# Kernel optimization log

Hardware: AMD Instinct MI355X
Metric: run time of the kernel (lower is better)

## Reference

```python
import jax, jax.numpy as jnp
import numpy as np

N_USER, N_ITEM = 100000, 50000
D, H, B, E = 64, 64, 16384, 2000000

def _xavier(key, shape):
    fan_in, fan_out = shape[0], shape[1]
    lim = float(np.sqrt(6.0 / (fan_in + fan_out)))
    return jax.random.uniform(key, shape, jnp.float32, -lim, lim)

def setup_inputs() -> dict:
    key = jax.random.key(0)
    ks = jax.random.split(key, 16)
    inp = {
        "user_table": _xavier(ks[0], (N_USER, D)),
        "item_table": _xavier(ks[1], (N_ITEM, D)),
        "Wu": _xavier(ks[2], (D, D)),   # GCN_user weight ([in,out])
        "bu": jnp.zeros((D,), jnp.float32),
        "Wi": _xavier(ks[3], (D, D)),   # GCN_item weight
        "bi": jnp.zeros((D,), jnp.float32),
        "W1": _xavier(ks[4], (4 * D, 2 * H)),
        "b1": jnp.zeros((2 * H,), jnp.float32),
        "W2": _xavier(ks[5], (2 * H, H)),
        "b2": jnp.zeros((H,), jnp.float32),
        "W3": _xavier(ks[6], (H, 1)),
        "b3": jnp.zeros((1,), jnp.float32),
        "user_bias": jnp.zeros((N_USER, 1), jnp.float32),
        "item_bias": jnp.zeros((N_ITEM, 1), jnp.float32),
        "user_id": jax.random.randint(ks[7], (B,), 0, N_USER),
        "item_id": jax.random.randint(ks[8], (B,), 0, N_ITEM),
        "edge_user": jax.random.randint(ks[9], (E,), 0, N_USER),
        "edge_item": jax.random.randint(ks[10], (E,), 0, N_ITEM),
    }
    return inp

def reference(user_table, item_table, Wu, bu, Wi, bi, W1, b1, W2, b2, W3, b3,
              user_bias, item_bias, user_id, item_id, edge_user, edge_item):
    # sparse.mm(edge_ui, item_h)[user_id]: aggregate item embeddings per user
    agg_i = jax.ops.segment_sum(item_table[edge_item], edge_user, num_segments=N_USER)[user_id]
    agg_u = jax.ops.segment_sum(user_table[edge_user], edge_item, num_segments=N_ITEM)[item_id]
    ones_e = jnp.ones((edge_user.shape[0],), jnp.float32)
    deg_u = jax.ops.segment_sum(ones_e, edge_user, num_segments=N_USER)[user_id] + 1.0  # item_din
    deg_i = jax.ops.segment_sum(ones_e, edge_item, num_segments=N_ITEM)[item_id] + 1.0  # user_din
    gcn_item_h = agg_i / deg_u[:, None]   # [B, D]
    gcn_user_h = agg_u / deg_i[:, None]   # [B, D]
    # dropout p=0.3 is identity in eval mode
    gcn_user_out = jax.nn.relu(gcn_user_h @ Wu + bu)
    gcn_item_out = jax.nn.relu(gcn_item_h @ Wi + bi)
    u_emb = user_table[user_id]
    i_emb = item_table[item_id]
    x = jnp.concatenate([u_emb * i_emb,
                         u_emb * gcn_item_out,
                         gcn_user_out * i_emb,
                         gcn_user_out * gcn_item_out], axis=-1)  # [B, 4D]
    x1 = jnp.tanh(x @ W1 + b1)
    x2 = jnp.tanh(x1 @ W2 + b2)
    x3 = (x2 @ W3 + b3).reshape(-1)
    return x3 + user_bias[user_id, 0] + item_bias[item_id, 0]
```

## Files before the change

### kernel.cpp

```cpp
#include <hip/hip_runtime.h>
#include <cstdint>
#include <cstddef>

#define D 64
#define CAPU 96
#define CAPI 128
#define OCAP 4096
#define GR 32

__global__ __launch_bounds__(256) void k_build_maps(const int* __restrict__ user_id,
                                                    const int* __restrict__ item_id,
                                                    int* __restrict__ map_u,
                                                    int* __restrict__ map_i, int B)
{
    int i = blockIdx.x * blockDim.x + threadIdx.x;
    if (i < B) {
        atomicCAS(&map_u[user_id[i]], -1, i);
        atomicCAS(&map_i[item_id[i]], -1, i);
    }
}

__global__ __launch_bounds__(256) void k_scatter(const int* __restrict__ edge_user,
                                                 const int* __restrict__ edge_item,
                                                 const int* __restrict__ map_u,
                                                 const int* __restrict__ map_i,
                                                 int* __restrict__ cntU,
                                                 int* __restrict__ cntI,
                                                 uint32_t* __restrict__ listU,
                                                 uint32_t* __restrict__ listI,
                                                 int* __restrict__ ovfCnt,
                                                 uint32_t* __restrict__ ovf, int E)
{
    int t = blockIdx.x * blockDim.x + threadIdx.x;
    int base = t * 2;
    if (base >= E) return;

    int u0, u1 = -1, i0, i1 = 0;
    if (base + 2 <= E) {
        int2 eu = *(const int2*)(edge_user + base);
        int2 ei = *(const int2*)(edge_item + base);
        u0 = eu.x; u1 = eu.y; i0 = ei.x; i1 = ei.y;
    } else {
        u0 = edge_user[base]; i0 = edge_item[base];
    }

    int su0 = map_u[u0];
    int si0 = map_i[i0];
    int su1 = (u1 >= 0) ? map_u[u1] : -1;
    int si1 = (u1 >= 0) ? map_i[i1] : -1;

    if (su0 >= 0) {
        int pos = atomicAdd(&cntU[su0 * 16], 1);
        if (pos < CAPU) listU[(size_t)su0 * CAPU + pos] = (uint32_t)i0;
        else { int o = atomicAdd(ovfCnt, 1);
               if (o < OCAP) ovf[o] = ((uint32_t)su0 << 17) | (uint32_t)i0; }
    }
    if (si0 >= 0) {
        int pos = atomicAdd(&cntI[si0 * 16], 1);
        if (pos < CAPI) listI[(size_t)si0 * CAPI + pos] = (uint32_t)u0;
        else { int o = atomicAdd(ovfCnt, 1);
               if (o < OCAP) ovf[o] = 0x80000000u | ((uint32_t)si0 << 17) | (uint32_t)u0; }
    }
    if (su1 >= 0) {
        int pos = atomicAdd(&cntU[su1 * 16], 1);
        if (pos < CAPU) listU[(size_t)su1 * CAPU + pos] = (uint32_t)i1;
        else { int o = atomicAdd(ovfCnt, 1);
               if (o < OCAP) ovf[o] = ((uint32_t)su1 << 17) | (uint32_t)i1; }
    }
    if (si1 >= 0) {
        int pos = atomicAdd(&cntI[si1 * 16], 1);
        if (pos < CAPI) listI[(size_t)si1 * CAPI + pos] = (uint32_t)u1;
        else { int o = atomicAdd(ovfCnt, 1);
               if (o < OCAP) ovf[o] = 0x80000000u | ((uint32_t)si1 << 17) | (uint32_t)u1; }
    }
}

__global__ __launch_bounds__(256) void k_gather(const uint32_t* __restrict__ listU,
                                                const uint32_t* __restrict__ listI,
                                                const int* __restrict__ cntU,
                                                const int* __restrict__ cntI,
                                                const float* __restrict__ user_table,
                                                const float* __restrict__ item_table,
                                                const int* __restrict__ ovfCnt,
                                                const uint32_t* __restrict__ ovf,
                                                float* __restrict__ aggIU,
                                                float* __restrict__ aggUI, int B)
{
    int gg = (blockIdx.x * blockDim.x + threadIdx.x) >> 4;
    if (gg >= 2 * B) return;
    int l16 = threadIdx.x & 15;
    int side = gg >= B;
    int slot = side ? gg - B : gg;

    int cnt = side ? cntI[slot * 16] : cntU[slot * 16];
    int caps = side ? CAPI : CAPU;
    int n = cnt < caps ? cnt : caps;
    const uint32_t* list = side ? (listI + (size_t)slot * CAPI)
                                : (listU + (size_t)slot * CAPU);
    const float4* table4 = (const float4*)(side ? user_table : item_table);

    float4 a0 = {0.f,0.f,0.f,0.f}, a1 = {0.f,0.f,0.f,0.f};
    float4 a2 = {0.f,0.f,0.f,0.f}, a3 = {0.f,0.f,0.f,0.f};
    int j = 0;
    for (; j + 4 <= n; j += 4) {
        int r0 = (int)list[j], r1 = (int)list[j+1], r2 = (int)list[j+2], r3 = (int)list[j+3];
        float4 v0 = table4[(size_t)r0 * 16 + l16];
        float4 v1 = table4[(size_t)r1 * 16 + l16];
        float4 v2 = table4[(size_t)r2 * 16 + l16];
        float4 v3 = table4[(size_t)r3 * 16 + l16];
        a0.x += v0.x; a0.y += v0.y; a0.z += v0.z; a0.w += v0.w;
        a1.x += v1.x; a1.y += v1.y; a1.z += v1.z; a1.w += v1.w;
        a2.x += v2.x; a2.y += v2.y; a2.z += v2.z; a2.w += v2.w;
        a3.x += v3.x; a3.y += v3.y; a3.z += v3.z; a3.w += v3.w;
    }
    for (; j < n; ++j) {
        int r0 = (int)list[j];
        float4 v0 = table4[(size_t)r0 * 16 + l16];
        a0.x += v0.x; a0.y += v0.y; a0.z += v0.z; a0.w += v0.w;
    }
    if (cnt > caps) {
        int on = *ovfCnt; if (on > OCAP) on = OCAP;
        for (int k = 0; k < on; ++k) {
            uint32_t p = ovf[k];
            if ((int)(p >> 31) == side && (int)((p >> 17) & 0x3FFFu) == slot) {
                float4 v = table4[(size_t)(p & 0x1FFFFu) * 16 + l16];
                a0.x += v.x; a0.y += v.y; a0.z += v.z; a0.w += v.w;
            }
        }
    }
    float inv = 1.0f / ((float)cnt + 1.0f);
    float4 acc = {(a0.x+a1.x+a2.x+a3.x) * inv, (a0.y+a1.y+a2.y+a3.y) * inv,
                  (a0.z+a1.z+a2.z+a3.z) * inv, (a0.w+a1.w+a2.w+a3.w) * inv};
    float4* agg4 = (float4*)(side ? aggUI : aggIU);
    agg4[(size_t)slot * 16 + l16] = acc;
}

__global__ __launch_bounds__(256) void k_gcn_mlp(const int* __restrict__ user_id,
                                                 const int* __restrict__ item_id,
                                                 const int* __restrict__ map_u,
                                                 const int* __restrict__ map_i,
                                                 const float* __restrict__ aggIU,
                                                 const float* __restrict__ aggUI,
                                                 const float* __restrict__ user_table,
                                                 const float* __restrict__ item_table,
                                                 const float* __restrict__ Wi,
                                                 const float* __restrict__ bi,
                                                 const float* __restrict__ Wu,
                                                 const float* __restrict__ bu,
                                                 const float* __restrict__ W1,
                                                 const float* __restrict__ b1,
                                                 const float* __restrict__ W2,
                                                 const float* __restrict__ b2,
                                                 const float* __restrict__ W3,
                                                 const float* __restrict__ b3,
                                                 const float* __restrict__ user_bias,
                                                 const float* __restrict__ item_bias,
                                                 float* __restrict__ out, int B)
{
    __shared__ float XgiL[GR][68];
    __shared__ float XguL[GR][68];
    __shared__ float Fbuf[2 * GR][68];
    __shared__ float WB[8192];
    __shared__ int sU[GR], sI[GR];
    int t = threadIdx.x;
    int row0 = blockIdx.x * GR;
    if (t < GR) { sU[t] = user_id[row0 + t]; sI[t] = item_id[row0 + t]; }
    __syncthreads();

    int txg = t & 15, tyg = t >> 4;
    {
        const float4* agg4 = (const float4*)aggIU;
        #pragma unroll
        for (int q = 0; q < 2; ++q) {
            int idx = t * 2 + q; int r = idx >> 4, l16 = idx & 15;
            int slot = map_u[sU[r]];
            ((float4*)&Fbuf[r][0])[l16] = agg4[(size_t)slot * 16 + l16];
        }
        const float4* wg = (const float4*)Wi;
        float4* d = (float4*)WB;
        #pragma unroll
        for (int q = 0; q < 4; ++q) d[t + q * 256] = wg[t + q * 256];
    }
    __syncthreads();
    {
        float acc[2][4] = {};
        for (int k = 0; k < 64; ++k) {
            float a0 = Fbuf[2 * tyg][k], a1 = Fbuf[2 * tyg + 1][k];
            #pragma unroll
            for (int c = 0; c < 4; ++c) {
                float w = WB[k * 64 + txg + 16 * c];
                acc[0][c] = fmaf(a0, w, acc[0][c]);
                acc[1][c] = fmaf(a1, w, acc[1][c]);
            }
        }
        #pragma unroll
        for (int r = 0; r < 2; ++r)
            #pragma unroll
            for (int c = 0; c < 4; ++c)
                XgiL[2 * tyg + r][txg + 16 * c] = fmaxf(acc[r][c] + bi[txg + 16 * c], 0.f);
    }
    __syncthreads();
    {
        const float4* agg4 = (const float4*)aggUI;
        #pragma unroll
        for (int q = 0; q < 2; ++q) {
            int idx = t * 2 + q; int r = idx >> 4, l16 = idx & 15;
            int slot = map_i[sI[r]];
            ((float4*)&Fbuf[r][0])[l16] = agg4[(size_t)slot * 16 + l16];
        }
        const float4* wg = (const float4*)Wu;
        float4* d = (float4*)WB;
        #pragma unroll
        for (int q = 0; q < 4; ++q) d[t + q * 256] = wg[t + q * 256];
    }
    __syncthreads();
    {
        float acc[2][4] = {};
        for (int k = 0; k < 64; ++k) {
            float a0 = Fbuf[2 * tyg][k], a1 = Fbuf[2 * tyg + 1][k];
            #pragma unroll
            for (int c = 0; c < 4; ++c) {
                float w = WB[k * 64 + txg + 16 * c];
                acc[0][c] = fmaf(a0, w, acc[0][c]);
                acc[1][c] = fmaf(a1, w, acc[1][c]);
            }
        }
        #pragma unroll
        for (int r = 0; r < 2; ++r)
            #pragma unroll
            for (int c = 0; c < 4; ++c)
                XguL[2 * tyg + r][txg + 16 * c] = fmaxf(acc[r][c] + bu[txg + 16 * c], 0.f);
    }
    __syncthreads();

    #pragma unroll
    for (int q = 0; q < 2; ++q) {
        int idx = t * 2 + q; int r = idx >> 4, l16 = idx & 15;
        ((float4*)&Fbuf[r][0])[l16] = ((const float4*)user_table)[(size_t)sU[r] * 16 + l16];
        ((float4*)&Fbuf[GR + r][0])[l16] = ((const float4*)item_table)[(size_t)sI[r] * 16 + l16];
    }

    int tx1 = t & 31, ty1 = t >> 5;
    float acc1[4][4] = {};
    for (int j = 0; j < 4; ++j) {
        {
            const float4* w4 = (const float4*)W1 + (size_t)j * 2048;
            float4* d = (float4*)WB;
            #pragma unroll
            for (int q = 0; q < 8; ++q) d[t + q * 256] = w4[t + q * 256];
        }
        __syncthreads();
        const float (*FA)[68] = (j < 2) ? (const float (*)[68])&Fbuf[0] : (const float (*)[68])XguL;
        const float (*FB)[68] = ((j & 1) == 0) ? (const float (*)[68])&Fbuf[GR] : (const float (*)[68])XgiL;
        for (int k = 0; k < 64; ++k) {
            float a[4], b[4];
            #pragma unroll
            for (int r = 0; r < 4; ++r) a[r] = FA[4 * ty1 + r][k] * FB[4 * ty1 + r][k];
            #pragma unroll
            for (int c = 0; c < 4; ++c) b[c] = WB[k * 128 + tx1 + 32 * c];
            #pragma unroll
            for (int r = 0; r < 4; ++r)
                #pragma unroll
                for (int c = 0; c < 4; ++c)
                    acc1[r][c] = fmaf(a[r], b[c], acc1[r][c]);
        }
        __syncthreads();
    }

    float* x1t = &Fbuf[0][0];
    #pragma unroll
    for (int r = 0; r < 4; ++r)
        #pragma unroll
        for (int c = 0; c < 4; ++c) {
            int col = tx1 + 32 * c;
            x1t[(4 * ty1 + r) * 132 + col] = tanhf(acc1[r][c] + b1[col]);
        }
    {
        const float4* w4 = (const float4*)W2;
        float4* d = (float4*)WB;
        #pragma unroll
        for (int q = 0; q < 8; ++q) d[t + q * 256] = w4[t + q * 256];
    }
    __syncthreads();

    int tx2 = t & 15, ty2 = t >> 4;
    float acc2[2][4] = {};
    for (int k = 0; k < 128; ++k) {
        float a0 = x1t[(2 * ty2) * 132 + k];
        float a1 = x1t[(2 * ty2 + 1) * 132 + k];
        #pragma unroll
        for (int c = 0; c < 4; ++c) {
            float w = WB[k * 64 + tx2 + 16 * c];
            acc2[0][c] = fmaf(a0, w, acc2[0][c]);
            acc2[1][c] = fmaf(a1, w, acc2[1][c]);
        }
    }
    float b3v = b3[0];
    #pragma unroll
    for (int r = 0; r < 2; ++r) {
        int lr = 2 * ty2 + r;
        float p = 0.f;
        #pragma unroll
        for (int c = 0; c < 4; ++c) {
            int col = tx2 + 16 * c;
            p += tanhf(acc2[r][c] + b2[col]) * W3[col];
        }
        p += __shfl_xor(p, 1);
        p += __shfl_xor(p, 2);
        p += __shfl_xor(p, 4);
        p += __shfl_xor(p, 8);
        if (tx2 == 0)
            out[row0 + lr] = p + b3v + user_bias[sU[lr]] + item_bias[sI[lr]];
    }
}

extern "C" void kernel_launch(void* const* d_in, const int* in_sizes, int n_in,
                              void* d_out, int out_size, void* d_ws, size_t ws_size,
                              hipStream_t stream)
{
    const float* user_table = (const float*)d_in[0];
    const float* item_table = (const float*)d_in[1];
    const float* Wu = (const float*)d_in[2];
    const float* bu = (const float*)d_in[3];
    const float* Wi = (const float*)d_in[4];
    const float* bi = (const float*)d_in[5];
    const float* W1 = (const float*)d_in[6];
    const float* b1 = (const float*)d_in[7];
    const float* W2 = (const float*)d_in[8];
    const float* b2 = (const float*)d_in[9];
    const float* W3 = (const float*)d_in[10];
    const float* b3 = (const float*)d_in[11];
    const float* user_bias = (const float*)d_in[12];
    const float* item_bias = (const float*)d_in[13];
    const int* user_id = (const int*)d_in[14];
    const int* item_id = (const int*)d_in[15];
    const int* edge_user = (const int*)d_in[16];
    const int* edge_item = (const int*)d_in[17];

    const int N_USER = in_sizes[0] / D;
    const int N_ITEM = in_sizes[1] / D;
    const int B = in_sizes[14];
    const int E = in_sizes[16];

    char* ws = (char*)d_ws;
    size_t off = 0;
    const size_t aggIU_off = off; off += (size_t)B * D * 4;
    const size_t aggUI_off = off; off += (size_t)B * D * 4;
    const size_t mapu_off  = off; off += (size_t)N_USER * 4;
    const size_t mapi_off  = off; off += (size_t)N_ITEM * 4;
    const size_t cntU_off  = off; off += (size_t)B * 16 * 4;
    const size_t cntI_off  = off; off += (size_t)B * 16 * 4;
    const size_t ovfc_off  = off; off += 256;
    const size_t ovf_off   = off; off += (size_t)OCAP * 4;
    const size_t listU_off = off; off += (size_t)B * CAPU * 4;
    const size_t listI_off = off; off += (size_t)B * CAPI * 4;

    float* aggIU = (float*)(ws + aggIU_off);
    float* aggUI = (float*)(ws + aggUI_off);
    int*   map_u = (int*)(ws + mapu_off);
    int*   map_i = (int*)(ws + mapi_off);
    int*   cntU  = (int*)(ws + cntU_off);
    int*   cntI  = (int*)(ws + cntI_off);
    int*   ovfCnt = (int*)(ws + ovfc_off);
    uint32_t* ovf = (uint32_t*)(ws + ovf_off);
    uint32_t* listU = (uint32_t*)(ws + listU_off);
    uint32_t* listI = (uint32_t*)(ws + listI_off);

    hipMemsetAsync(ws + mapu_off, 0xFF, (size_t)(N_USER + N_ITEM) * 4, stream);
    hipMemsetAsync(ws + cntU_off, 0, (size_t)B * 16 * 4 * 2 + 256 + OCAP * 4, stream);

    k_build_maps<<<(B + 255) / 256, 256, 0, stream>>>(user_id, item_id, map_u, map_i, B);

    k_scatter<<<(E / 2 + 255) / 256, 256, 0, stream>>>(edge_user, edge_item, map_u, map_i,
                                                       cntU, cntI, listU, listI, ovfCnt, ovf, E);

    k_gather<<<(2 * B) / 16, 256, 0, stream>>>(listU, listI, cntU, cntI,
                                               user_table, item_table, ovfCnt, ovf,
                                               aggIU, aggUI, B);

    k_gcn_mlp<<<B / GR, 256, 0, stream>>>(user_id, item_id, map_u, map_i,
                                          aggIU, aggUI, user_table, item_table,
                                          Wi, bi, Wu, bu, W1, b1, W2, b2, W3, b3,
                                          user_bias, item_bias, (float*)d_out, B);
}
```

Measured before the change: 238.4 us.

## Partition edge scatter by slot range across block groups for atomic locality

The scatter kernel becomes a grid-stride loop over 2048 blocks split into 8 partitions. Every partition reads all edges with 16-byte nontemporal loads, but each one only does atomics and list writes for batch slots in its own 2048-slot range. The goal is to keep each block group's atomic counters and list rows within a smaller memory footprint so they get better cache locality. In exchange, the edge arrays and map lookups are read 8 times, and the leftover tail edges are handled by a single block.

```diff
diff --git a/kernel.cpp b/kernel.cpp
--- a/kernel.cpp
+++ b/kernel.cpp
@@ -7,6 +7,10 @@
 #define CAPI 128
 #define OCAP 4096
 #define GR 32
+#define NPART 8
+#define PSHIFT 11
+
+typedef int v4i __attribute__((ext_vector_type(4)));
 
 __global__ __launch_bounds__(256) void k_build_maps(const int* __restrict__ user_id,
                                                     const int* __restrict__ item_id,
@@ -31,47 +35,53 @@
                                                  int* __restrict__ ovfCnt,
                                                  uint32_t* __restrict__ ovf, int E)
 {
-    int t = blockIdx.x * blockDim.x + threadIdx.x;
-    int base = t * 2;
-    if (base >= E) return;
-
-    int u0, u1 = -1, i0, i1 = 0;
-    if (base + 2 <= E) {
-        int2 eu = *(const int2*)(edge_user + base);
-        int2 ei = *(const int2*)(edge_item + base);
-        u0 = eu.x; u1 = eu.y; i0 = ei.x; i1 = ei.y;
-    } else {
-        u0 = edge_user[base]; i0 = edge_item[base];
-    }
-
-    int su0 = map_u[u0];
-    int si0 = map_i[i0];
-    int su1 = (u1 >= 0) ? map_u[u1] : -1;
-    int si1 = (u1 >= 0) ? map_i[i1] : -1;
-
-    if (su0 >= 0) {
-        int pos = atomicAdd(&cntU[su0 * 16], 1);
-        if (pos < CAPU) listU[(size_t)su0 * CAPU + pos] = (uint32_t)i0;
-        else { int o = atomicAdd(ovfCnt, 1);
-               if (o < OCAP) ovf[o] = ((uint32_t)su0 << 17) | (uint32_t)i0; }
-    }
-    if (si0 >= 0) {
-        int pos = atomicAdd(&cntI[si0 * 16], 1);
-        if (pos < CAPI) listI[(size_t)si0 * CAPI + pos] = (uint32_t)u0;
-        else { int o = atomicAdd(ovfCnt, 1);
-               if (o < OCAP) ovf[o] = 0x80000000u | ((uint32_t)si0 << 17) | (uint32_t)u0; }
-    }
-    if (su1 >= 0) {
-        int pos = atomicAdd(&cntU[su1 * 16], 1);
-        if (pos < CAPU) listU[(size_t)su1 * CAPU + pos] = (uint32_t)i1;
-        else { int o = atomicAdd(ovfCnt, 1);
-               if (o < OCAP) ovf[o] = ((uint32_t)su1 << 17) | (uint32_t)i1; }
-    }
-    if (si1 >= 0) {
-        int pos = atomicAdd(&cntI[si1 * 16], 1);
-        if (pos < CAPI) listI[(size_t)si1 * CAPI + pos] = (uint32_t)u1;
-        else { int o = atomicAdd(ovfCnt, 1);
-               if (o < OCAP) ovf[o] = 0x80000000u | ((uint32_t)si1 << 17) | (uint32_t)u1; }
+    const int part = blockIdx.x & (NPART - 1);
+    const int nb = gridDim.x >> 3;
+    const int bc = blockIdx.x >> 3;
+    const int tid = threadIdx.x;
+    const int nquads = E >> 2;
+
+    for (int q = bc * 256 + tid; q < nquads; q += nb * 256) {
+        int base = q * 4;
+        v4i eu = __builtin_nontemporal_load((const v4i*)(edge_user + base));
+        v4i ei = __builtin_nontemporal_load((const v4i*)(edge_item + base));
+        #pragma unroll
+        for (int k = 0; k < 4; ++k) {
+            int u = eu[k], it = ei[k];
+            int su = map_u[u];
+            int si = map_i[it];
+            if ((su >> PSHIFT) == part) {
+                int pos = atomicAdd(&cntU[su * 16], 1);
+                if (pos < CAPU) listU[(size_t)su * CAPU + pos] = (uint32_t)it;
+                else { int o = atomicAdd(ovfCnt, 1);
+                       if (o < OCAP) ovf[o] = ((uint32_t)su << 17) | (uint32_t)it; }
+            }
+            if ((si >> PSHIFT) == part) {
+                int pos = atomicAdd(&cntI[si * 16], 1);
+                if (pos < CAPI) listI[(size_t)si * CAPI + pos] = (uint32_t)u;
+                else { int o = atomicAdd(ovfCnt, 1);
+                       if (o < OCAP) ovf[o] = 0x80000000u | ((uint32_t)si << 17) | (uint32_t)u; }
+            }
+        }
+    }
+
+    if (part == 0 && bc == 0) {
+        for (int e = (nquads << 2) + tid; e < E; e += 256) {
+            int u = edge_user[e], it = edge_item[e];
+            int su = map_u[u], si = map_i[it];
+            if (su >= 0) {
+                int pos = atomicAdd(&cntU[su * 16], 1);
+                if (pos < CAPU) listU[(size_t)su * CAPU + pos] = (uint32_t)it;
+                else { int o = atomicAdd(ovfCnt, 1);
+                       if (o < OCAP) ovf[o] = ((uint32_t)su << 17) | (uint32_t)it; }
+            }
+            if (si >= 0) {
+                int pos = atomicAdd(&cntI[si * 16], 1);
+                if (pos < CAPI) listI[(size_t)si * CAPI + pos] = (uint32_t)u;
+                else { int o = atomicAdd(ovfCnt, 1);
+                       if (o < OCAP) ovf[o] = 0x80000000u | ((uint32_t)si << 17) | (uint32_t)u; }
+            }
+        }
     }
 }
 
@@ -371,8 +381,8 @@
 
     k_build_maps<<<(B + 255) / 256, 256, 0, stream>>>(user_id, item_id, map_u, map_i, B);
 
-    k_scatter<<<(E / 2 + 255) / 256, 256, 0, stream>>>(edge_user, edge_item, map_u, map_i,
-                                                       cntU, cntI, listU, listI, ovfCnt, ovf, E);
+    k_scatter<<<2048, 256, 0, stream>>>(edge_user, edge_item, map_u, map_i,
+                                        cntU, cntI, listU, listI, ovfCnt, ovf, E);
 
     k_gather<<<(2 * B) / 16, 256, 0, stream>>>(listU, listI, cntU, cntI,
                                                user_table, item_table, ovfCnt, ovf,
```

New measurement: 378.4 us. 1.59x slower.
